# Optimization experiments

Measured on AMD Instinct MI355X. Metric: run time of the kernel, lower is better.

The kernel has to match this reference:

```python
import jax, jax.numpy as jnp
import numpy as np

D = 1024
H = 16
DK = D // H


def setup_inputs() -> dict:
    key = jax.random.key(0)
    ks = jax.random.split(key, 10)
    B, S = 2, 2048
    scale = 1.0 / np.sqrt(D)
    inp = {
        "x": jax.random.normal(ks[0], (B, S, D), dtype=jnp.float32),
        "mask": jax.random.randint(ks[1], (B, S), 0, 2, dtype=jnp.int32),
        "wq": jax.random.normal(ks[2], (D, D), dtype=jnp.float32) * scale,
        "bq": jnp.zeros((D,), dtype=jnp.float32),
        "wk": jax.random.normal(ks[3], (D, D), dtype=jnp.float32) * scale,
        "bk": jnp.zeros((D,), dtype=jnp.float32),
        "wv": jax.random.normal(ks[4], (D, D), dtype=jnp.float32) * scale,
        "bv": jnp.zeros((D,), dtype=jnp.float32),
        "wo": jax.random.normal(ks[5], (D, D), dtype=jnp.float32) * scale,
        "bo": jnp.zeros((D,), dtype=jnp.float32),
    }
    return inp


def reference(x, mask, wq, bq, wk, bk, wv, bv, wo, bo):
    B, S, _ = x.shape
    # torch Linear: y = x @ W.T + b
    def proj(w, b):
        return (jnp.einsum("bsd,ed->bse", x, w) + b).reshape(B, S, H, DK).transpose(0, 2, 1, 3)  # (B,H,S,dk)

    q = proj(wq, bq)
    k = proj(wk, bk)
    v = proj(wv, bv)

    scores = jnp.einsum("bhqd,bhkd->bhqk", q, k) / jnp.sqrt(jnp.float32(DK))  # (B,H,S,S)
    # original: mask.unsqueeze(1).unsqueeze(3) -> (B,1,S,1), masks along the QUERY axis
    m = mask[:, None, :, None]  # (B,1,S,1)
    scores = jnp.where(m == 0, jnp.float32(-1e9), scores)
    attn = jax.nn.softmax(scores, axis=-1)
    ctx = jnp.einsum("bhqk,bhkd->bhqd", attn, v)  # (B,H,S,dk)
    concat = ctx.transpose(0, 2, 1, 3).reshape(B, S, D)
    return jnp.einsum("bsd,ed->bse", concat, wo) + bo
```

## Files before the change

kernel.cpp:

```cpp
#include <hip/hip_runtime.h>
#include <hip/hip_bf16.h>

#define SEQ 2048
#define DM  1024

typedef __attribute__((ext_vector_type(8))) _Float16 f16x8;
typedef __attribute__((ext_vector_type(4)))  float   f32x4;

#define EXP2F(x) __builtin_amdgcn_exp2f(x)

__device__ __forceinline__ ushort f2h(float x) {
    union { _Float16 h; ushort u; } c; c.h = (_Float16)x; return c.u;
}
__device__ __forceinline__ unsigned pk2h(float a, float b) {
    typedef __fp16 fp16v2 __attribute__((ext_vector_type(2)));
    union { fp16v2 h; unsigned u; } c;
    c.h = __builtin_amdgcn_cvt_pkrtz(a, b);
    return c.u;
}

__device__ __forceinline__ void gload16(const void* g, void* l) {
    __builtin_amdgcn_global_load_lds(
        (const __attribute__((address_space(1))) unsigned*)(uintptr_t)g,
        (__attribute__((address_space(3))) unsigned*)(uintptr_t)l, 16, 0, 0);
}

__global__ __launch_bounds__(256)
void cvt_all(const float* __restrict__ x,  const float* __restrict__ wq,
             const float* __restrict__ wk, const float* __restrict__ wv,
             const float* __restrict__ wo,
             ushort* __restrict__ xH, ushort* __restrict__ wH)
{
    const int NX4 = (2 * SEQ * DM) / 4;
    const int NW4 = (DM * DM) / 4;
    const int total = NX4 + 4 * NW4;
    for (int i = blockIdx.x * 256 + threadIdx.x; i < total; i += gridDim.x * 256) {
        float4 v; ushort4* dst;
        if (i < NX4) {
            v = ((const float4*)x)[i];
            dst = (ushort4*)xH + i;
        } else {
            const int j = i - NX4;
            const int wi = j >> 18;
            const int jo = j & (NW4 - 1);
            const float* ws_ = (wi == 0) ? wq : (wi == 1) ? wk : (wi == 2) ? wv : wo;
            v = ((const float4*)ws_)[jo];
            dst = (ushort4*)wH + j;
        }
        ushort4 h;
        h.x = f2h(v.x); h.y = f2h(v.y); h.z = f2h(v.z); h.w = f2h(v.w);
        *dst = h;
    }
}

template<int BM, int BN, int WM, int WN, int MODE>
__global__ __launch_bounds__(WM * WN * 64)
void gemm5(const ushort* __restrict__ A, const ushort* __restrict__ B,
           const float* __restrict__ b0, const float* __restrict__ b1,
           const float* __restrict__ b2,
           ushort* __restrict__ QH, ushort* __restrict__ KH,
           ushort* __restrict__ VH, float* __restrict__ outf, int nmt)
{
    constexpr int NW  = WM * WN;
    constexpr int PR  = BM / WM, PC = BN / WN;
    constexpr int MR  = PR / 16, NR = PC / 16, MH = MR / 2;
    constexpr int APW = (BM / 8) / NW;
    constexpr int BPW = (BN / 8) / NW;
    constexpr int NT  = DM / 64;

    __shared__ ushort A_lds[2][BM * 64];
    __shared__ ushort B_lds[2][BN * 64];

    const int tid = threadIdx.x, w = tid >> 6, lane = tid & 63;
    const int nwg = gridDim.x, q8 = nwg >> 3;
    const int wg  = (blockIdx.x & 7) * q8 + (blockIdx.x >> 3);
    const int m0  = (wg % nmt) * BM, n0 = (wg / nmt) * BN;
    const int wm  = w / WN, wn = w % WN;

    auto stage = [&](int buf, int kt) {
        const int k0 = kt * 64;
#pragma unroll
        for (int j = 0; j < APW; ++j) {
            const int s   = w * APW + j;
            const int row = s * 8 + (lane >> 3);
            const int cl  = (lane & 7) ^ (row & 7);
            gload16(A + (size_t)(m0 + row) * DM + k0 + cl * 8,
                    &A_lds[buf][s * 512]);
        }
#pragma unroll
        for (int j = 0; j < BPW; ++j) {
            const int s   = w * BPW + j;
            const int row = s * 8 + (lane >> 3);
            const int cl  = (lane & 7) ^ (row & 7);
            gload16(B + (size_t)(n0 + row) * DM + k0 + cl * 8,
                    &B_lds[buf][s * 512]);
        }
    };

    f32x4 acc[MR][NR];
#pragma unroll
    for (int i = 0; i < MR; ++i)
#pragma unroll
        for (int j = 0; j < NR; ++j) acc[i][j] = f32x4{0.f, 0.f, 0.f, 0.f};

    stage(0, 0);
    stage(1, 1);

    for (int t = 0; t < NT; ++t) {
        const int buf = t & 1;
        if (t == NT - 1) asm volatile("s_waitcnt vmcnt(0)" ::: "memory");
        else             asm volatile("s_waitcnt vmcnt(8)" ::: "memory");
        __builtin_amdgcn_sched_barrier(0);
        __builtin_amdgcn_s_barrier();

        f16x8 bf_[NR][2];
#pragma unroll
        for (int nf = 0; nf < NR; ++nf) {
            const int r = wn * PC + nf * 16 + (lane & 15);
#pragma unroll
            for (int kb = 0; kb < 2; ++kb) {
                const int c = kb * 4 + (lane >> 4);
                bf_[nf][kb] = *(const f16x8*)&B_lds[buf][r * 64 + ((c ^ (r & 7)) << 3)];
            }
        }
#pragma unroll
        for (int qm = 0; qm < 2; ++qm) {
            f16x8 af_[MH][2];
#pragma unroll
            for (int mf = 0; mf < MH; ++mf) {
                const int r = wm * PR + qm * (PR / 2) + mf * 16 + (lane & 15);
#pragma unroll
                for (int kb = 0; kb < 2; ++kb) {
                    const int c = kb * 4 + (lane >> 4);
                    af_[mf][kb] = *(const f16x8*)&A_lds[buf][r * 64 + ((c ^ (r & 7)) << 3)];
                }
            }
            __builtin_amdgcn_s_setprio(1);
#pragma unroll
            for (int kb = 0; kb < 2; ++kb)
#pragma unroll
                for (int mf = 0; mf < MH; ++mf)
#pragma unroll
                    for (int nf = 0; nf < NR; ++nf)
                        acc[qm * MH + mf][nf] = __builtin_amdgcn_mfma_f32_16x16x32_f16(
                            af_[mf][kb], bf_[nf][kb], acc[qm * MH + mf][nf], 0, 0, 0);
            __builtin_amdgcn_s_setprio(0);
        }
        __builtin_amdgcn_sched_barrier(0);
        __builtin_amdgcn_s_barrier();
        __builtin_amdgcn_sched_barrier(0);
        if (t + 2 < NT) stage(buf, t + 2);
    }

#pragma unroll
    for (int mf = 0; mf < MR; ++mf)
#pragma unroll
        for (int nf = 0; nf < NR; ++nf) {
            const int col  = n0 + wn * PC + nf * 16 + (lane & 15);
            const int row0 = m0 + wm * PR + mf * 16 + ((lane >> 4) << 2);
            f32x4 v = acc[mf][nf];
            if constexpr (MODE == 1) {
                float4 o;
                o.x = v[0] + b0[row0 + 0];
                o.y = v[1] + b0[row0 + 1];
                o.z = v[2] + b0[row0 + 2];
                o.w = v[3] + b0[row0 + 3];
                *(float4*)&outf[(size_t)col * DM + row0] = o;
            } else {
                const int sel = row0 >> 10;
                const int e = row0 & 1023;
                const int b = col >> 11, s = col & 2047;
                const int h = e >> 6, dk = e & 63;
                const float* bp = (sel == 0) ? b0 : (sel == 1) ? b1 : b2;
                const float sc = (sel == 0) ? 0.125f * 1.44269504089f : 1.0f;
                const float v0 = (v[0] + bp[e + 0]) * sc;
                const float v1 = (v[1] + bp[e + 1]) * sc;
                const float v2 = (v[2] + bp[e + 2]) * sc;
                const float v3 = (v[3] + bp[e + 3]) * sc;
                const int bh = b * 16 + h;
                ushort4 hv;
                hv.x = f2h(v0); hv.y = f2h(v1); hv.z = f2h(v2); hv.w = f2h(v3);
                if (sel == 0) {
                    const size_t off = ((size_t)bh * SEQ + s) * 64 + dk;
                    *(ushort4*)&QH[off] = hv;
                } else if (sel == 1) {
                    const size_t off = ((size_t)bh * SEQ + s) * 64 + dk;
                    *(ushort4*)&KH[off] = hv;
                } else {
                    const size_t o0 = ((size_t)bh * 64 + dk) * SEQ + s;
                    VH[o0]           = hv.x;
                    VH[o0 + SEQ]     = hv.y;
                    VH[o0 + 2 * SEQ] = hv.z;
                    VH[o0 + 3 * SEQ] = hv.w;
                }
            }
        }
}

__global__ __launch_bounds__(512, 3)
void attn_k(const ushort* __restrict__ QH, const ushort* __restrict__ KH,
            const ushort* __restrict__ VH, const int* __restrict__ mask,
            ushort* __restrict__ ch)
{
    __shared__ ushort Ks[2][64 * 64];
    __shared__ ushort Vs[2][64 * 64];
    __shared__ ushort Ps[8][16 * 64];

    const int t = threadIdx.x, w = t >> 6, lane = t & 63;
    const int wg = (blockIdx.x & 7) * 64 + (blockIdx.x >> 3);
    const int bh = wg >> 4, qt = wg & 15;
    const int b = bh >> 4, h = bh & 15;
    const int q0 = qt * 128 + w * 16;
    const size_t base = (size_t)bh * SEQ * 64;
    const int lq = lane & 15, cb = lane >> 4;

    const int msk = mask[b * SEQ + q0 + lq];
    f16x8 qf[2];
#pragma unroll
    for (int kb = 0; kb < 2; ++kb) {
        qf[kb] = *(const f16x8*)&QH[base + (size_t)(q0 + lq) * 64 + kb * 32 + cb * 8];
        if (msk == 0) qf[kb] = f16x8{0, 0, 0, 0, 0, 0, 0, 0};
    }

    float l_run = 0.f;
    f32x4 acc[4];
#pragma unroll
    for (int df = 0; df < 4; ++df) acc[df] = f32x4{0.f, 0.f, 0.f, 0.f};

    f16x8 sK, sV;
    const int sr = t >> 3, scc = t & 7;
    const int wr_off = sr * 64 + (scc ^ (sr & 7)) * 8;
    const ushort* gK = &KH[base + (size_t)sr * 64 + scc * 8];
    const ushort* gV = &VH[base + (size_t)sr * SEQ + scc * 8];
    auto stage_load = [&]() {
        sK = *(const f16x8*)gK;
        sV = *(const f16x8*)gV;
        gK += 4096;
        gV += 64;
    };

    stage_load();
    *(f16x8*)&Ks[0][wr_off] = sK;
    *(f16x8*)&Vs[0][wr_off] = sV;
    stage_load();
    __syncthreads();

    auto body = [&](const int BUF, const bool WR, const bool LD) {
        if (WR) {
            *(f16x8*)&Ks[BUF ^ 1][wr_off] = sK;
            *(f16x8*)&Vs[BUF ^ 1][wr_off] = sV;
        }
        if (LD) stage_load();

        f32x4 st[4];
#pragma unroll
        for (int mf = 0; mf < 4; ++mf) st[mf] = f32x4{0.f, 0.f, 0.f, 0.f};
        __builtin_amdgcn_s_setprio(1);
#pragma unroll
        for (int mf = 0; mf < 4; ++mf) {
            const int r = mf * 16 + lq;
#pragma unroll
            for (int kb = 0; kb < 2; ++kb) {
                const int p = (kb * 4 + cb) ^ (r & 7);
                f16x8 kf = *(const f16x8*)&Ks[BUF][r * 64 + p * 8];
                st[mf] = __builtin_amdgcn_mfma_f32_16x16x32_f16(kf, qf[kb], st[mf], 0, 0, 0);
            }
        }
        __builtin_amdgcn_s_setprio(0);

        float parts[4];
#pragma unroll
        for (int mf = 0; mf < 4; ++mf) {
            const float e0 = EXP2F(st[mf][0]);
            const float e1 = EXP2F(st[mf][1]);
            const float e2 = EXP2F(st[mf][2]);
            const float e3 = EXP2F(st[mf][3]);
            parts[mf] = (e0 + e1) + (e2 + e3);
            uint2 pw;
            pw.x = pk2h(e0, e1);
            pw.y = pk2h(e2, e3);
            const int key0 = mf * 16 + (cb << 2);
            const int p = (key0 >> 3) ^ (lq & 7);
            *(uint2*)&Ps[w][lq * 64 + p * 8 + (key0 & 7)] = pw;
        }
        float ss = (parts[0] + parts[1]) + (parts[2] + parts[3]);
        ss += __shfl_xor(ss, 16);
        ss += __shfl_xor(ss, 32);
        l_run += ss;

        f16x8 pf[2];
#pragma unroll
        for (int kb = 0; kb < 2; ++kb) {
            const int p = (kb * 4 + cb) ^ (lq & 7);
            pf[kb] = *(const f16x8*)&Ps[w][lq * 64 + p * 8];
        }
        __builtin_amdgcn_s_setprio(1);
#pragma unroll
        for (int df = 0; df < 4; ++df) {
            const int r = df * 16 + lq;
#pragma unroll
            for (int kb = 0; kb < 2; ++kb) {
                const int p = (kb * 4 + cb) ^ (r & 7);
                f16x8 vf = *(const f16x8*)&Vs[BUF][r * 64 + p * 8];
                acc[df] = __builtin_amdgcn_mfma_f32_16x16x32_f16(vf, pf[kb], acc[df], 0, 0, 0);
            }
        }
        __builtin_amdgcn_s_setprio(0);

        __syncthreads();
    };

#pragma unroll 1
    for (int i = 0; i < 15; ++i) {
        body(0, true, true);
        body(1, true, true);
    }
    body(0, true, false);
    body(1, false, false);

    {
        const float inv = 1.0f / l_run;
        const int s = q0 + lq;
#pragma unroll
        for (int df = 0; df < 4; ++df) {
            const int e0 = h * 64 + df * 16 + (cb << 2);
            ushort4 hv;
            hv.x = f2h(acc[df][0] * inv);
            hv.y = f2h(acc[df][1] * inv);
            hv.z = f2h(acc[df][2] * inv);
            hv.w = f2h(acc[df][3] * inv);
            *(ushort4*)&ch[(size_t)(b * SEQ + s) * DM + e0] = hv;
        }
    }
}

extern "C" void kernel_launch(void* const* d_in, const int* in_sizes, int n_in,
                              void* d_out, int out_size, void* d_ws, size_t ws_size,
                              hipStream_t stream)
{
    const float* x  = (const float*)d_in[0];
    const int* mask = (const int*)d_in[1];
    const float* wq = (const float*)d_in[2];
    const float* bq = (const float*)d_in[3];
    const float* wk = (const float*)d_in[4];
    const float* bk = (const float*)d_in[5];
    const float* wv = (const float*)d_in[6];
    const float* bv = (const float*)d_in[7];
    const float* wo = (const float*)d_in[8];
    const float* bo = (const float*)d_in[9];
    float* out = (float*)d_out;

    const size_t M1 = 1024 * 1024;
    ushort* W = (ushort*)d_ws;
    ushort* xH = W;
    ushort* wH = W + 4 * M1;
    ushort* QH = W + 8 * M1;
    ushort* KH = W + 12 * M1;
    ushort* VH = W + 16 * M1;

    cvt_all<<<2048, 256, 0, stream>>>(x, wq, wk, wv, wo, xH, wH);

    gemm5<384, 128, 4, 2, 0><<<256, 512, 0, stream>>>(
        wH, xH, bq, bk, bv, QH, KH, VH, nullptr, 8);

    attn_k<<<512, 512, 0, stream>>>(QH, KH, VH, mask, xH);

    gemm5<128, 128, 2, 2, 1><<<256, 256, 0, stream>>>(
        wH + 3 * M1, xH, bo, nullptr, nullptr,
        nullptr, nullptr, nullptr, out, 8);
}
```

Baseline: 105.6 us.

## Halve attention block size and interleave exp with PV MFMA halves

The attention kernel now runs 1024 blocks of 256 threads (64 queries per block) instead of 512 blocks of 512 threads, so each thread stages two K/V rows per tile. Within the loop body, the softmax exponentials for the first half of the keys are written to LDS and consumed by PV MFMAs before the second half is computed. This is meant to overlap transcendental/VALU work with matrix work and to improve scheduling granularity. In exchange, each K/V tile is loaded twice as often across blocks, since fewer queries share it.

New measurement: 112.6 us. +6.7%, slower.

```diff
diff --git a/kernel.cpp b/kernel.cpp
--- a/kernel.cpp
+++ b/kernel.cpp
@@ -197,20 +197,20 @@
         }
 }
 
-__global__ __launch_bounds__(512, 3)
+__global__ __launch_bounds__(256, 4)
 void attn_k(const ushort* __restrict__ QH, const ushort* __restrict__ KH,
             const ushort* __restrict__ VH, const int* __restrict__ mask,
             ushort* __restrict__ ch)
 {
     __shared__ ushort Ks[2][64 * 64];
     __shared__ ushort Vs[2][64 * 64];
-    __shared__ ushort Ps[8][16 * 64];
+    __shared__ ushort Ps[4][16 * 64];
 
     const int t = threadIdx.x, w = t >> 6, lane = t & 63;
-    const int wg = (blockIdx.x & 7) * 64 + (blockIdx.x >> 3);
-    const int bh = wg >> 4, qt = wg & 15;
+    const int wg = (blockIdx.x & 7) * 128 + (blockIdx.x >> 3);
+    const int bh = wg >> 5, qt = wg & 31;
     const int b = bh >> 4, h = bh & 15;
-    const int q0 = qt * 128 + w * 16;
+    const int q0 = qt * 64 + w * 16;
     const size_t base = (size_t)bh * SEQ * 64;
     const int lq = lane & 15, cb = lane >> 4;
 
@@ -227,28 +227,31 @@
 #pragma unroll
     for (int df = 0; df < 4; ++df) acc[df] = f32x4{0.f, 0.f, 0.f, 0.f};
 
-    f16x8 sK, sV;
-    const int sr = t >> 3, scc = t & 7;
-    const int wr_off = sr * 64 + (scc ^ (sr & 7)) * 8;
-    const ushort* gK = &KH[base + (size_t)sr * 64 + scc * 8];
-    const ushort* gV = &VH[base + (size_t)sr * SEQ + scc * 8];
+    f16x8 sK0, sV0, sK1, sV1;
+    const int sr0 = t >> 3, sr1 = sr0 + 32, scc = t & 7;
+    const int wr0 = sr0 * 64 + (scc ^ (sr0 & 7)) * 8;
+    const int wr1 = sr1 * 64 + (scc ^ (sr1 & 7)) * 8;
+    const ushort* gK0 = &KH[base + (size_t)sr0 * 64 + scc * 8];
+    const ushort* gK1 = &KH[base + (size_t)sr1 * 64 + scc * 8];
+    const ushort* gV0 = &VH[base + (size_t)sr0 * SEQ + scc * 8];
+    const ushort* gV1 = &VH[base + (size_t)sr1 * SEQ + scc * 8];
     auto stage_load = [&]() {
-        sK = *(const f16x8*)gK;
-        sV = *(const f16x8*)gV;
-        gK += 4096;
-        gV += 64;
+        sK0 = *(const f16x8*)gK0;  sK1 = *(const f16x8*)gK1;
+        sV0 = *(const f16x8*)gV0;  sV1 = *(const f16x8*)gV1;
+        gK0 += 4096; gK1 += 4096;
+        gV0 += 64;   gV1 += 64;
     };
 
     stage_load();
-    *(f16x8*)&Ks[0][wr_off] = sK;
-    *(f16x8*)&Vs[0][wr_off] = sV;
+    *(f16x8*)&Ks[0][wr0] = sK0;  *(f16x8*)&Ks[0][wr1] = sK1;
+    *(f16x8*)&Vs[0][wr0] = sV0;  *(f16x8*)&Vs[0][wr1] = sV1;
     stage_load();
     __syncthreads();
 
     auto body = [&](const int BUF, const bool WR, const bool LD) {
         if (WR) {
-            *(f16x8*)&Ks[BUF ^ 1][wr_off] = sK;
-            *(f16x8*)&Vs[BUF ^ 1][wr_off] = sV;
+            *(f16x8*)&Ks[BUF ^ 1][wr0] = sK0;  *(f16x8*)&Ks[BUF ^ 1][wr1] = sK1;
+            *(f16x8*)&Vs[BUF ^ 1][wr0] = sV0;  *(f16x8*)&Vs[BUF ^ 1][wr1] = sV1;
         }
         if (LD) stage_load();
 
@@ -270,7 +273,7 @@
 
         float parts[4];
 #pragma unroll
-        for (int mf = 0; mf < 4; ++mf) {
+        for (int mf = 0; mf < 2; ++mf) {
             const float e0 = EXP2F(st[mf][0]);
             const float e1 = EXP2F(st[mf][1]);
             const float e2 = EXP2F(st[mf][2]);
@@ -283,29 +286,50 @@
             const int p = (key0 >> 3) ^ (lq & 7);
             *(uint2*)&Ps[w][lq * 64 + p * 8 + (key0 & 7)] = pw;
         }
+        {
+            const int p0 = cb ^ (lq & 7);
+            f16x8 pf0 = *(const f16x8*)&Ps[w][lq * 64 + p0 * 8];
+            __builtin_amdgcn_s_setprio(1);
+#pragma unroll
+            for (int df = 0; df < 4; ++df) {
+                const int r = df * 16 + lq;
+                const int p = cb ^ (r & 7);
+                f16x8 vf = *(const f16x8*)&Vs[BUF][r * 64 + p * 8];
+                acc[df] = __builtin_amdgcn_mfma_f32_16x16x32_f16(vf, pf0, acc[df], 0, 0, 0);
+            }
+            __builtin_amdgcn_s_setprio(0);
+        }
+#pragma unroll
+        for (int mf = 2; mf < 4; ++mf) {
+            const float e0 = EXP2F(st[mf][0]);
+            const float e1 = EXP2F(st[mf][1]);
+            const float e2 = EXP2F(st[mf][2]);
+            const float e3 = EXP2F(st[mf][3]);
+            parts[mf] = (e0 + e1) + (e2 + e3);
+            uint2 pw;
+            pw.x = pk2h(e0, e1);
+            pw.y = pk2h(e2, e3);
+            const int key0 = mf * 16 + (cb << 2);
+            const int p = (key0 >> 3) ^ (lq & 7);
+            *(uint2*)&Ps[w][lq * 64 + p * 8 + (key0 & 7)] = pw;
+        }
+        {
+            const int p1 = (4 + cb) ^ (lq & 7);
+            f16x8 pf1 = *(const f16x8*)&Ps[w][lq * 64 + p1 * 8];
+            __builtin_amdgcn_s_setprio(1);
+#pragma unroll
+            for (int df = 0; df < 4; ++df) {
+                const int r = df * 16 + lq;
+                const int p = (4 + cb) ^ (r & 7);
+                f16x8 vf = *(const f16x8*)&Vs[BUF][r * 64 + p * 8];
+                acc[df] = __builtin_amdgcn_mfma_f32_16x16x32_f16(vf, pf1, acc[df], 0, 0, 0);
+            }
+            __builtin_amdgcn_s_setprio(0);
+        }
         float ss = (parts[0] + parts[1]) + (parts[2] + parts[3]);
         ss += __shfl_xor(ss, 16);
         ss += __shfl_xor(ss, 32);
         l_run += ss;
-
-        f16x8 pf[2];
-#pragma unroll
-        for (int kb = 0; kb < 2; ++kb) {
-            const int p = (kb * 4 + cb) ^ (lq & 7);
-            pf[kb] = *(const f16x8*)&Ps[w][lq * 64 + p * 8];
-        }
-        __builtin_amdgcn_s_setprio(1);
-#pragma unroll
-        for (int df = 0; df < 4; ++df) {
-            const int r = df * 16 + lq;
-#pragma unroll
-            for (int kb = 0; kb < 2; ++kb) {
-                const int p = (kb * 4 + cb) ^ (r & 7);
-                f16x8 vf = *(const f16x8*)&Vs[BUF][r * 64 + p * 8];
-                acc[df] = __builtin_amdgcn_mfma_f32_16x16x32_f16(vf, pf[kb], acc[df], 0, 0, 0);
-            }
-        }
-        __builtin_amdgcn_s_setprio(0);
 
         __syncthreads();
     };
@@ -363,7 +387,7 @@
     gemm5<384, 128, 4, 2, 0><<<256, 512, 0, stream>>>(
         wH, xH, bq, bk, bv, QH, KH, VH, nullptr, 8);
 
-    attn_k<<<512, 512, 0, stream>>>(QH, KH, VH, mask, xH);
+    attn_k<<<1024, 256, 0, stream>>>(QH, KH, VH, mask, xH);
 
     gemm5<128, 128, 2, 2, 1><<<256, 256, 0, stream>>>(
         wH + 3 * M1, xH, bo, nullptr, nullptr,
```

## Split softmax exp and PV MFMA into halves; defer row-sum reduction to epilogue

Applied to the files above, without the earlier changes.

The per-tile softmax is split into two halves: exp and P-store for the first 32 keys, then the PV MFMAs for that half, then the second half. This lets exp work interleave with matrix ops. The cross-lane row-sum shuffle moves out of the loop into the final normalization, which removes two shuffles per tile. Launch bounds drop from 3 to 2 waves per SIMD, giving the compiler more registers at the cost of occupancy.

After: 104.1 us. Within noise of the previous version (-1.4%).

```diff
diff --git a/kernel.cpp b/kernel.cpp
--- a/kernel.cpp
+++ b/kernel.cpp
@@ -197,7 +197,7 @@
         }
 }
 
-__global__ __launch_bounds__(512, 3)
+__global__ __launch_bounds__(512, 2)
 void attn_k(const ushort* __restrict__ QH, const ushort* __restrict__ KH,
             const ushort* __restrict__ VH, const int* __restrict__ mask,
             ushort* __restrict__ ch)
@@ -222,7 +222,7 @@
         if (msk == 0) qf[kb] = f16x8{0, 0, 0, 0, 0, 0, 0, 0};
     }
 
-    float l_run = 0.f;
+    float l_part = 0.f;
     f32x4 acc[4];
 #pragma unroll
     for (int df = 0; df < 4; ++df) acc[df] = f32x4{0.f, 0.f, 0.f, 0.f};
@@ -268,14 +268,13 @@
         }
         __builtin_amdgcn_s_setprio(0);
 
-        float parts[4];
-#pragma unroll
-        for (int mf = 0; mf < 4; ++mf) {
+#pragma unroll
+        for (int mf = 0; mf < 2; ++mf) {
             const float e0 = EXP2F(st[mf][0]);
             const float e1 = EXP2F(st[mf][1]);
             const float e2 = EXP2F(st[mf][2]);
             const float e3 = EXP2F(st[mf][3]);
-            parts[mf] = (e0 + e1) + (e2 + e3);
+            l_part += (e0 + e1) + (e2 + e3);
             uint2 pw;
             pw.x = pk2h(e0, e1);
             pw.y = pk2h(e2, e3);
@@ -283,29 +282,46 @@
             const int p = (key0 >> 3) ^ (lq & 7);
             *(uint2*)&Ps[w][lq * 64 + p * 8 + (key0 & 7)] = pw;
         }
-        float ss = (parts[0] + parts[1]) + (parts[2] + parts[3]);
-        ss += __shfl_xor(ss, 16);
-        ss += __shfl_xor(ss, 32);
-        l_run += ss;
-
-        f16x8 pf[2];
-#pragma unroll
-        for (int kb = 0; kb < 2; ++kb) {
-            const int p = (kb * 4 + cb) ^ (lq & 7);
-            pf[kb] = *(const f16x8*)&Ps[w][lq * 64 + p * 8];
-        }
-        __builtin_amdgcn_s_setprio(1);
-#pragma unroll
-        for (int df = 0; df < 4; ++df) {
-            const int r = df * 16 + lq;
-#pragma unroll
-            for (int kb = 0; kb < 2; ++kb) {
-                const int p = (kb * 4 + cb) ^ (r & 7);
+        {
+            const int p0 = cb ^ (lq & 7);
+            f16x8 pf0 = *(const f16x8*)&Ps[w][lq * 64 + p0 * 8];
+            __builtin_amdgcn_s_setprio(1);
+#pragma unroll
+            for (int df = 0; df < 4; ++df) {
+                const int r = df * 16 + lq;
+                const int p = cb ^ (r & 7);
                 f16x8 vf = *(const f16x8*)&Vs[BUF][r * 64 + p * 8];
-                acc[df] = __builtin_amdgcn_mfma_f32_16x16x32_f16(vf, pf[kb], acc[df], 0, 0, 0);
-            }
-        }
-        __builtin_amdgcn_s_setprio(0);
+                acc[df] = __builtin_amdgcn_mfma_f32_16x16x32_f16(vf, pf0, acc[df], 0, 0, 0);
+            }
+            __builtin_amdgcn_s_setprio(0);
+        }
+#pragma unroll
+        for (int mf = 2; mf < 4; ++mf) {
+            const float e0 = EXP2F(st[mf][0]);
+            const float e1 = EXP2F(st[mf][1]);
+            const float e2 = EXP2F(st[mf][2]);
+            const float e3 = EXP2F(st[mf][3]);
+            l_part += (e0 + e1) + (e2 + e3);
+            uint2 pw;
+            pw.x = pk2h(e0, e1);
+            pw.y = pk2h(e2, e3);
+            const int key0 = mf * 16 + (cb << 2);
+            const int p = (key0 >> 3) ^ (lq & 7);
+            *(uint2*)&Ps[w][lq * 64 + p * 8 + (key0 & 7)] = pw;
+        }
+        {
+            const int p1 = (4 + cb) ^ (lq & 7);
+            f16x8 pf1 = *(const f16x8*)&Ps[w][lq * 64 + p1 * 8];
+            __builtin_amdgcn_s_setprio(1);
+#pragma unroll
+            for (int df = 0; df < 4; ++df) {
+                const int r = df * 16 + lq;
+                const int p = (4 + cb) ^ (r & 7);
+                f16x8 vf = *(const f16x8*)&Vs[BUF][r * 64 + p * 8];
+                acc[df] = __builtin_amdgcn_mfma_f32_16x16x32_f16(vf, pf1, acc[df], 0, 0, 0);
+            }
+            __builtin_amdgcn_s_setprio(0);
+        }
 
         __syncthreads();
     };
@@ -319,7 +335,10 @@
     body(1, false, false);
 
     {
-        const float inv = 1.0f / l_run;
+        float l_tot = l_part;
+        l_tot += __shfl_xor(l_tot, 16);
+        l_tot += __shfl_xor(l_tot, 32);
+        const float inv = 1.0f / l_tot;
         const int s = q0 + lq;
 #pragma unroll
         for (int df = 0; df < 4; ++df) {
```
